# Kernel optimization log

Hardware: AMD Instinct MI355X
Metric: run time of the kernel (lower is better)

Reference implementation:

```python
import jax, jax.numpy as jnp
import numpy as np

B, N, D, H = 8, 1024, 512, 512  # batch, nodes/graph, input dim, hidden/output dim
NEG_SLOPE = 0.2


def _gatv2_layer(x, src, dst, Wl, bl, Wr, br, a, bias, nseg):
    """PyG GATv2Conv (heads=1, add_self_loops=False, eval mode -> no dropout).
    message j->i: alpha_ij = softmax_i( a . leaky_relu(xl[j] + xr[i]) ); out[i] = sum_j alpha_ij * xl[j] + bias
    """
    xl = x @ Wl + bl              # [nseg, H] source transform
    xr = x @ Wr + br              # [nseg, H] target transform
    e = jax.nn.leaky_relu(xl[src] + xr[dst], NEG_SLOPE) @ a  # [E] raw scores
    m = jax.lax.stop_gradient(jax.ops.segment_max(e, dst, num_segments=nseg))
    ex = jnp.exp(e - m[dst])
    s = jax.ops.segment_sum(ex, dst, num_segments=nseg)
    alpha = ex / s[dst]                                       # segment softmax over incoming edges
    out = jax.ops.segment_sum(alpha[:, None] * xl[src], dst, num_segments=nseg)
    return out + bias


def setup_inputs() -> dict:
    key = jax.random.key(0)
    rng = np.random.RandomState(0)
    # random per-graph adjacency, avg degree ~16; block-diagonal edge extraction
    adj_np = (rng.rand(B, N, N) < (16.0 / N))
    srcs, dsts = [], []
    for b in range(B):  # matches torch.nonzero(big_adj).t(): row=src, col=dst
        r, c = np.nonzero(adj_np[b])
        srcs.append(r + b * N)
        dsts.append(c + b * N)
    edge_index = jnp.asarray(np.stack([np.concatenate(srcs), np.concatenate(dsts)]).astype(np.int32))

    ks = jax.random.split(key, 32)
    def lin(k, fi, fo):
        return (jax.random.normal(k, (fi, fo), jnp.float32) / np.sqrt(fi)).astype(jnp.float32)
    inp = {
        "batch_graph": jax.random.normal(ks[0], (B, N, D), jnp.float32),
        "adj": jnp.asarray(adj_np.astype(np.float32)),
        "edge_index": edge_index,
    }
    dims = [(D, H), (H, H), (H, H)]
    for i, (fi, fo) in enumerate(dims, start=1):
        k = jax.random.split(ks[i], 6)
        inp[f"Wl{i}"] = lin(k[0], fi, fo)
        inp[f"bl{i}"] = jnp.zeros((fo,), jnp.float32)
        inp[f"Wr{i}"] = lin(k[1], fi, fo)
        inp[f"br{i}"] = jnp.zeros((fo,), jnp.float32)
        inp[f"a{i}"] = (jax.random.normal(k[2], (fo,), jnp.float32) / np.sqrt(fo)).astype(jnp.float32)
        inp[f"bias{i}"] = jnp.zeros((fo,), jnp.float32)
    return inp


def reference(batch_graph, adj, edge_index,
              Wl1, bl1, Wr1, br1, a1, bias1,
              Wl2, bl2, Wr2, br2, a2, bias2,
              Wl3, bl3, Wr3, br3, a3, bias3):
    b, n, d = batch_graph.shape
    nseg = b * n
    x = batch_graph.reshape(nseg, d)
    src, dst = edge_index[0], edge_index[1]
    x = _gatv2_layer(x, src, dst, Wl1, bl1, Wr1, br1, a1, bias1, nseg)  # graph_norm = Identity
    x = _gatv2_layer(x, src, dst, Wl2, bl2, Wr2, br2, a2, bias2, nseg)
    x = _gatv2_layer(x, src, dst, Wl3, bl3, Wr3, br3, a3, bias3, nseg)
    return x.reshape(b, n, -1)
```

## Files before the change

kernel.cpp:

```cpp
#include <hip/hip_runtime.h>
#include <math.h>

#define MTOT 8192
#define HD   512

typedef __attribute__((ext_vector_type(8))) short bf16x8;
typedef __attribute__((ext_vector_type(4))) float floatx4;
typedef __attribute__((ext_vector_type(4))) float f32x4;
typedef __attribute__((ext_vector_type(4))) unsigned short u16x4;

__device__ inline unsigned short f2bf(float f) {
    unsigned int u = __float_as_uint(f);
    unsigned int r = (u + 0x7FFFu + ((u >> 16) & 1u)) >> 16;
    return (unsigned short)r;
}
__device__ inline float bf2f(unsigned short h) {
    return __uint_as_float(((unsigned int)h) << 16);
}

__device__ inline void nt_st4(float* p, float4 v) {
    f32x4 t = {v.x, v.y, v.z, v.w};
    __builtin_nontemporal_store(t, (f32x4*)p);
}
__device__ inline void nt_stu4(unsigned short* p, ushort4 v) {
    u16x4 t = {v.x, v.y, v.z, v.w};
    __builtin_nontemporal_store(t, (u16x4*)p);
}
__device__ inline float4 nt_ld4(const float* p) {
    f32x4 v = __builtin_nontemporal_load((const f32x4*)p);
    return make_float4(v.x, v.y, v.z, v.w);
}

__device__ inline float wave_sum64(float v) {
    int t;
    t = __builtin_amdgcn_update_dpp(0, __float_as_int(v), 0x121, 0xF, 0xF, true); v += __int_as_float(t);
    t = __builtin_amdgcn_update_dpp(0, __float_as_int(v), 0x122, 0xF, 0xF, true); v += __int_as_float(t);
    t = __builtin_amdgcn_update_dpp(0, __float_as_int(v), 0x124, 0xF, 0xF, true); v += __int_as_float(t);
    t = __builtin_amdgcn_update_dpp(0, __float_as_int(v), 0x128, 0xF, 0xF, true); v += __int_as_float(t);
    v += __shfl_xor(v, 16, 64);
    v += __shfl_xor(v, 32, 64);
    return v;
}


__global__ void count_deg(const int* __restrict__ dst, int* __restrict__ deg, int E) {
    int i = blockIdx.x * 256 + threadIdx.x;
    if (i < E) atomicAdd(&deg[dst[i]], 1);
}

__global__ __launch_bounds__(1024) void scan_offsets(const int* __restrict__ deg,
                                                     int* __restrict__ offs,
                                                     int* __restrict__ cursor) {
    __shared__ int part[1024];
    int tid = threadIdx.x;
    int base = tid * 8;
    int v[8]; int s = 0;
    #pragma unroll
    for (int i = 0; i < 8; ++i) { v[i] = deg[base + i]; s += v[i]; }
    part[tid] = s;
    __syncthreads();
    for (int off = 1; off < 1024; off <<= 1) {
        int t = (tid >= off) ? part[tid - off] : 0;
        __syncthreads();
        part[tid] += t;
        __syncthreads();
    }
    int run = (tid == 0) ? 0 : part[tid - 1];
    #pragma unroll
    for (int i = 0; i < 8; ++i) {
        offs[base + i] = run;
        cursor[base + i] = run;
        run += v[i];
    }
    if (tid == 1023) offs[MTOT] = run;
}

__global__ void scatter_edges(const int* __restrict__ src, const int* __restrict__ dst,
                              int* __restrict__ cursor, int* __restrict__ csr_src, int E) {
    int i = blockIdx.x * 256 + threadIdx.x;
    if (i < E) {
        int p = atomicAdd(&cursor[dst[i]], 1);
        csr_src[p] = src[i];
    }
}


__global__ __launch_bounds__(256) void prep_convert(
    const float* __restrict__ W0, const float* __restrict__ W1,
    const float* __restrict__ W2, const float* __restrict__ W3,
    const float* __restrict__ W4, const float* __restrict__ W5,
    unsigned short* __restrict__ wtbase,
    const float* __restrict__ X,
    unsigned short* __restrict__ Ahi, unsigned short* __restrict__ Alo,
    int* __restrict__ deg)
{
    int z = blockIdx.z;
    if (z == 7) {
        if (blockIdx.x == 0 && blockIdx.y == 0)
            for (int i = threadIdx.x; i < MTOT; i += 256) deg[i] = 0;
        return;
    }
    if (z == 6) {
        int bid = blockIdx.x * 16 + blockIdx.y;
        int t0 = bid * 256 + threadIdx.x;
        #pragma unroll
        for (int it = 0; it < 16; ++it) {
            int i = (t0 + it * 65536) * 4;
            float4 vv = *(const float4*)(X + i);
            ushort4 h, l;
            h.x = f2bf(vv.x); l.x = f2bf(vv.x - bf2f(h.x));
            h.y = f2bf(vv.y); l.y = f2bf(vv.y - bf2f(h.y));
            h.z = f2bf(vv.z); l.z = f2bf(vv.z - bf2f(h.z));
            h.w = f2bf(vv.w); l.w = f2bf(vv.w - bf2f(h.w));
            *(ushort4*)(Ahi + i) = h;
            *(ushort4*)(Alo + i) = l;
        }
        return;
    }
    const float* W = (z == 0) ? W0 : (z == 1) ? W1 : (z == 2) ? W2
                   : (z == 3) ? W3 : (z == 4) ? W4 : W5;
    int L = z >> 1, lr = z & 1;
    const size_t SZ = (size_t)HD * HD;
    unsigned short* Whi = wtbase + (L * 4 + lr * 2) * SZ;
    unsigned short* Wlo = Whi + SZ;

    __shared__ float t[32][33];
    int bx = blockIdx.x * 32;
    int by = blockIdx.y * 32;
    int tx = threadIdx.x & 31, ty = threadIdx.x >> 5;
    for (int i = ty; i < 32; i += 8)
        t[i][tx] = W[(size_t)(by + i) * HD + bx + tx];
    __syncthreads();
    for (int i = ty; i < 32; i += 8) {
        float vv = t[tx][i];
        unsigned short h = f2bf(vv);
        unsigned short l = f2bf(vv - bf2f(h));
        Whi[(size_t)(bx + i) * HD + by + tx] = h;
        Wlo[(size_t)(bx + i) * HD + by + tx] = l;
    }
}


__global__ __launch_bounds__(256) void gemm_mfma_dual(
    const unsigned short* __restrict__ Ahi, const unsigned short* __restrict__ Alo,
    const unsigned short* __restrict__ Bhi_l, const unsigned short* __restrict__ Blo_l,
    const unsigned short* __restrict__ Bhi_r, const unsigned short* __restrict__ Blo_r,
    const float* __restrict__ bias_l, const float* __restrict__ bias_r,
    float* __restrict__ Cl, float* __restrict__ Cr)
{
    int bid = blockIdx.x;
    int virt = (bid & 7) * 64 + (bid >> 3);
    int g  = virt >> 3;
    int q  = virt & 7;
    int bz = q >> 2;
    int bm = g * 128, bn = (q & 3) * 128;

    const unsigned short* Bhi = bz ? Bhi_r : Bhi_l;
    const unsigned short* Blo = bz ? Blo_r : Blo_l;
    const float* bias         = bz ? bias_r : bias_l;
    float* C                  = bz ? Cr : Cl;

    __shared__ __align__(16) unsigned short lds[2][4 * 128 * 32];

    int tid = threadIdx.x;
    int wave = tid >> 6, lane = tid & 63;

    const unsigned short* gsrc[4] = {Ahi, Alo, Bhi, Blo};
    int rowbase[4] = {bm, bm, bn, bn};

    const unsigned short* gbase =
        gsrc[wave] + (size_t)(rowbase[wave] + (lane >> 2)) * 512 + (lane & 3) * 8;

    floatx4 acc[4][4] = {};

    int wm = wave & 1, wn = wave >> 1;
    int lr = lane & 15, lq = lane >> 4;

    #pragma unroll
    for (int rg = 0; rg < 8; ++rg) {
        __builtin_amdgcn_global_load_lds(
            (const __attribute__((address_space(1))) unsigned int*)(gbase + (size_t)rg * 16 * 512),
            (__attribute__((address_space(3))) unsigned int*)(&lds[0][wave * 4096 + rg * 512]),
            16, 0, 0);
    }
    __syncthreads();

    for (int it = 0; it < 16; ++it) {
        int cur = it & 1;
        if (it < 15) {
            const unsigned short* g2 = gbase + (it + 1) * 32;
            #pragma unroll
            for (int rg = 0; rg < 8; ++rg) {
                __builtin_amdgcn_global_load_lds(
                    (const __attribute__((address_space(1))) unsigned int*)(g2 + (size_t)rg * 16 * 512),
                    (__attribute__((address_space(3))) unsigned int*)(&lds[cur ^ 1][wave * 4096 + rg * 512]),
                    16, 0, 0);
            }
        }

        bf16x8 ah[4], al[4], bh[4], bl_[4];
        #pragma unroll
        for (int i = 0; i < 4; ++i) {
            int mrow = wm * 64 + i * 16 + lr;
            ah[i]  = *(const bf16x8*)&lds[cur][0 * 4096 + mrow * 32 + lq * 8];
            al[i]  = *(const bf16x8*)&lds[cur][1 * 4096 + mrow * 32 + lq * 8];
            int nrow = wn * 64 + i * 16 + lr;
            bh[i]  = *(const bf16x8*)&lds[cur][2 * 4096 + nrow * 32 + lq * 8];
            bl_[i] = *(const bf16x8*)&lds[cur][3 * 4096 + nrow * 32 + lq * 8];
        }
        #pragma unroll
        for (int i = 0; i < 4; ++i)
            #pragma unroll
            for (int j = 0; j < 4; ++j) {
                acc[i][j] = __builtin_amdgcn_mfma_f32_16x16x32_bf16(ah[i], bh[j],  acc[i][j], 0, 0, 0);
                acc[i][j] = __builtin_amdgcn_mfma_f32_16x16x32_bf16(ah[i], bl_[j], acc[i][j], 0, 0, 0);
                acc[i][j] = __builtin_amdgcn_mfma_f32_16x16x32_bf16(al[i], bh[j],  acc[i][j], 0, 0, 0);
            }

        __syncthreads();
    }

    #pragma unroll
    for (int j = 0; j < 4; ++j) {
        int n = bn + wn * 64 + j * 16 + lr;
        float bv = bias[n];
        #pragma unroll
        for (int i = 0; i < 4; ++i) {
            int mbase = bm + wm * 64 + i * 16 + lq * 4;
            #pragma unroll
            for (int r = 0; r < 4; ++r)
                C[(size_t)(mbase + r) * 512 + n] = acc[i][j][r] + bv;
        }
    }
}


#define DOT8(Xa, Xb, d0, d1)                                              \
    {                                                                     \
        float t_;                                                         \
        t_ = Xa.x + r0.x; d0 = fmaf(av0.x, t_, d0); d1 = fmaf(av0.x, fabsf(t_), d1); \
        t_ = Xa.y + r0.y; d0 = fmaf(av0.y, t_, d0); d1 = fmaf(av0.y, fabsf(t_), d1); \
        t_ = Xa.z + r0.z; d0 = fmaf(av0.z, t_, d0); d1 = fmaf(av0.z, fabsf(t_), d1); \
        t_ = Xa.w + r0.w; d0 = fmaf(av0.w, t_, d0); d1 = fmaf(av0.w, fabsf(t_), d1); \
        t_ = Xb.x + r1.x; d0 = fmaf(av1.x, t_, d0); d1 = fmaf(av1.x, fabsf(t_), d1); \
        t_ = Xb.y + r1.y; d0 = fmaf(av1.y, t_, d0); d1 = fmaf(av1.y, fabsf(t_), d1); \
        t_ = Xb.z + r1.z; d0 = fmaf(av1.z, t_, d0); d1 = fmaf(av1.z, fabsf(t_), d1); \
        t_ = Xb.w + r1.w; d0 = fmaf(av1.w, t_, d0); d1 = fmaf(av1.w, fabsf(t_), d1); \
    }

#define PROCESS4(Xa, Xb, q)                                               \
    {                                                                     \
        float pe[4];                                                      \
        _Pragma("unroll")                                                 \
        for (int k2 = 0; k2 < 4; ++k2) {                                  \
            float d0 = 0.f, d1 = 0.f;                                     \
            DOT8(Xa[k2], Xb[k2], d0, d1);                                 \
            pe[k2] = fmaf(0.6f, d0, 0.4f * d1);                           \
        }                                                                 \
        _Pragma("unroll")                                                 \
        for (int k2 = 0; k2 < 4; ++k2) pe[k2] = wave_sum64(pe[k2]);       \
        float e0 = pe[0];                                                 \
        float e1 = ((q) + 1 < ne) ? pe[1] : -3.0e38f;                     \
        float e2 = ((q) + 2 < ne) ? pe[2] : -3.0e38f;                     \
        float e3 = ((q) + 3 < ne) ? pe[3] : -3.0e38f;                     \
        float bm4 = fmaxf(fmaxf(e0, e1), fmaxf(e2, e3));                  \
        if (bm4 > m) {                                                    \
            float sc = __expf(m - bm4);                                   \
            s *= sc;                                                      \
            acc0.x *= sc; acc0.y *= sc; acc0.z *= sc; acc0.w *= sc;       \
            acc1.x *= sc; acc1.y *= sc; acc1.z *= sc; acc1.w *= sc;       \
            m = bm4;                                                      \
        }                                                                 \
        float w0 = __expf(e0 - m), w1 = __expf(e1 - m);                   \
        float w2 = __expf(e2 - m), w3 = __expf(e3 - m);                   \
        s += (w0 + w1) + (w2 + w3);                                       \
        acc0.x = fmaf(w0, Xa[0].x, fmaf(w1, Xa[1].x, fmaf(w2, Xa[2].x, fmaf(w3, Xa[3].x, acc0.x)))); \
        acc0.y = fmaf(w0, Xa[0].y, fmaf(w1, Xa[1].y, fmaf(w2, Xa[2].y, fmaf(w3, Xa[3].y, acc0.y)))); \
        acc0.z = fmaf(w0, Xa[0].z, fmaf(w1, Xa[1].z, fmaf(w2, Xa[2].z, fmaf(w3, Xa[3].z, acc0.z)))); \
        acc0.w = fmaf(w0, Xa[0].w, fmaf(w1, Xa[1].w, fmaf(w2, Xa[2].w, fmaf(w3, Xa[3].w, acc0.w)))); \
        acc1.x = fmaf(w0, Xb[0].x, fmaf(w1, Xb[1].x, fmaf(w2, Xb[2].x, fmaf(w3, Xb[3].x, acc1.x)))); \
        acc1.y = fmaf(w0, Xb[0].y, fmaf(w1, Xb[1].y, fmaf(w2, Xb[2].y, fmaf(w3, Xb[3].y, acc1.y)))); \
        acc1.z = fmaf(w0, Xb[0].z, fmaf(w1, Xb[1].z, fmaf(w2, Xb[2].z, fmaf(w3, Xb[3].z, acc1.z)))); \
        acc1.w = fmaf(w0, Xb[0].w, fmaf(w1, Xb[1].w, fmaf(w2, Xb[2].w, fmaf(w3, Xb[3].w, acc1.w)))); \
    }

__global__ __launch_bounds__(256, 4) void gat_online(
    const float* __restrict__ xl, const float* __restrict__ xr,
    const float* __restrict__ avec, const float* __restrict__ bias,
    const int* __restrict__ offs, const int* __restrict__ csr_src,
    float* __restrict__ out, unsigned short* __restrict__ Ohi,
    unsigned short* __restrict__ Olo, int write_fp32)
{
    int gid = blockIdx.x;
    int wv = threadIdx.x >> 6, lane = threadIdx.x & 63;
    int node = ((gid & 7) << 10) + ((gid >> 3) << 2) + wv;

    int nb = offs[node], ne = offs[node + 1];

    int jA[4], jB[4];
    int j0 = (nb < ne) ? csr_src[nb] : 0;
    jA[0] = j0;
    #pragma unroll
    for (int k = 1; k < 4; ++k) jA[k] = (nb + k < ne) ? csr_src[nb + k] : j0;
    #pragma unroll
    for (int k = 0; k < 4; ++k) jB[k] = (nb + 4 + k < ne) ? csr_src[nb + 4 + k] : j0;

    size_t loff = (size_t)lane * 8;
    size_t rowoff = (size_t)node * HD + loff;
    float4 r0 = nt_ld4(xr + rowoff);
    float4 r1 = nt_ld4(xr + rowoff + 4);
    float4 av0 = *(const float4*)(avec + loff);
    float4 av1 = *(const float4*)(avec + loff + 4);

    float m = -3.0e38f, s = 0.f;
    float4 acc0 = {0.f, 0.f, 0.f, 0.f}, acc1 = {0.f, 0.f, 0.f, 0.f};

    float4 Aa[4], Ab[4], Ba[4], Bb[4];
    #pragma unroll
    for (int k = 0; k < 4; ++k) {
        const float* xp = xl + (size_t)jA[k] * HD + loff;
        Aa[k] = *(const float4*)xp;
        Ab[k] = *(const float4*)(xp + 4);
    }

    int p = nb;
    if (p < ne) {
        for (;;) {
            #pragma unroll
            for (int k = 0; k < 4; ++k) {
                const float* xp = xl + (size_t)jB[k] * HD + loff;
                Ba[k] = *(const float4*)xp;
                Bb[k] = *(const float4*)(xp + 4);
            }
            {
                int p2 = p + 8;
                #pragma unroll
                for (int k = 0; k < 4; ++k)
                    jA[k] = (p2 + k < ne) ? csr_src[p2 + k] : j0;
            }
            PROCESS4(Aa, Ab, p);
            p += 4;
            if (p >= ne) break;

            #pragma unroll
            for (int k = 0; k < 4; ++k) {
                const float* xp = xl + (size_t)jA[k] * HD + loff;
                Aa[k] = *(const float4*)xp;
                Ab[k] = *(const float4*)(xp + 4);
            }
            {
                int p2 = p + 8;
                #pragma unroll
                for (int k = 0; k < 4; ++k)
                    jB[k] = (p2 + k < ne) ? csr_src[p2 + k] : j0;
            }
            PROCESS4(Ba, Bb, p);
            p += 4;
            if (p >= ne) break;
        }
    }

    float inv = (s > 0.f) ? 1.f / s : 0.f;
    float4 b0 = *(const float4*)(bias + loff);
    float4 b1 = *(const float4*)(bias + loff + 4);
    float4 o0, o1;
    o0.x = fmaf(acc0.x, inv, b0.x); o0.y = fmaf(acc0.y, inv, b0.y);
    o0.z = fmaf(acc0.z, inv, b0.z); o0.w = fmaf(acc0.w, inv, b0.w);
    o1.x = fmaf(acc1.x, inv, b1.x); o1.y = fmaf(acc1.y, inv, b1.y);
    o1.z = fmaf(acc1.z, inv, b1.z); o1.w = fmaf(acc1.w, inv, b1.w);

    if (write_fp32) {
        nt_st4(out + rowoff, o0);
        nt_st4(out + rowoff + 4, o1);
    } else {
        ushort4 h, lo;
        h.x = f2bf(o0.x); lo.x = f2bf(o0.x - bf2f(h.x));
        h.y = f2bf(o0.y); lo.y = f2bf(o0.y - bf2f(h.y));
        h.z = f2bf(o0.z); lo.z = f2bf(o0.z - bf2f(h.z));
        h.w = f2bf(o0.w); lo.w = f2bf(o0.w - bf2f(h.w));
        nt_stu4(Ohi + rowoff, h);
        nt_stu4(Olo + rowoff, lo);
        h.x = f2bf(o1.x); lo.x = f2bf(o1.x - bf2f(h.x));
        h.y = f2bf(o1.y); lo.y = f2bf(o1.y - bf2f(h.y));
        h.z = f2bf(o1.z); lo.z = f2bf(o1.z - bf2f(h.z));
        h.w = f2bf(o1.w); lo.w = f2bf(o1.w - bf2f(h.w));
        nt_stu4(Ohi + rowoff + 4, h);
        nt_stu4(Olo + rowoff + 4, lo);
    }
}


extern "C" void kernel_launch(void* const* d_in, const int* in_sizes, int n_in,
                              void* d_out, int out_size, void* d_ws, size_t ws_size,
                              hipStream_t stream) {
    const float* x0 = (const float*)d_in[0];
    const int* eidx = (const int*)d_in[2];
    int E = in_sizes[2] / 2;
    const int* esrc = eidx;
    const int* edst = eidx + E;

    const float* Wl[3] = {(const float*)d_in[3],  (const float*)d_in[9],  (const float*)d_in[15]};
    const float* bl[3] = {(const float*)d_in[4],  (const float*)d_in[10], (const float*)d_in[16]};
    const float* Wr[3] = {(const float*)d_in[5],  (const float*)d_in[11], (const float*)d_in[17]};
    const float* br[3] = {(const float*)d_in[6],  (const float*)d_in[12], (const float*)d_in[18]};
    const float* av[3] = {(const float*)d_in[7],  (const float*)d_in[13], (const float*)d_in[19]};
    const float* bs[3] = {(const float*)d_in[8],  (const float*)d_in[14], (const float*)d_in[20]};

    char* w = (char*)d_ws;
    unsigned short* Ahi = (unsigned short*)w; w += (size_t)MTOT * HD * 2;
    unsigned short* Alo = (unsigned short*)w; w += (size_t)MTOT * HD * 2;
    unsigned short* wtbase = (unsigned short*)w; w += 12 * (size_t)HD * HD * 2;
    float* xl = (float*)w; w += (size_t)MTOT * HD * 4;
    float* xr = (float*)w; w += (size_t)MTOT * HD * 4;
    int* deg    = (int*)w;
    int* offs   = deg + MTOT;
    int* cursor = offs + MTOT + 8;
    int* csr    = cursor + MTOT;
    const size_t SZ = (size_t)HD * HD;

    prep_convert<<<dim3(16, 16, 8), 256, 0, stream>>>(
        Wl[0], Wr[0], Wl[1], Wr[1], Wl[2], Wr[2], wtbase, x0, Ahi, Alo, deg);
    count_deg<<<(E + 255) / 256, 256, 0, stream>>>(edst, deg, E);
    scan_offsets<<<1, 1024, 0, stream>>>(deg, offs, cursor);
    scatter_edges<<<(E + 255) / 256, 256, 0, stream>>>(esrc, edst, cursor, csr, E);

    for (int L = 0; L < 3; ++L) {
        gemm_mfma_dual<<<512, 256, 0, stream>>>(Ahi, Alo,
            wtbase + (L * 4 + 0) * SZ, wtbase + (L * 4 + 1) * SZ,
            wtbase + (L * 4 + 2) * SZ, wtbase + (L * 4 + 3) * SZ,
            bl[L], br[L], xl, xr);
        int last = (L == 2);
        gat_online<<<MTOT / 4, 256, 0, stream>>>(xl, xr, av[L], bs[L], offs, csr,
                                                 last ? (float*)d_out : nullptr,
                                                 last ? nullptr : Ahi,
                                                 last ? nullptr : Alo,
                                                 last);
    }
}
```

Before: 301.4 us.

## Prefetch two stages ahead in GEMM with explicit vmcnt waits

Restructures the double-buffered GEMM main loop so two K-stages are issued up front and each later stage is launched after compute, two iterations ahead. It uses explicit s_waitcnt vmcnt counts plus raw s_barrier instead of __syncthreads, so only the loads for the current stage must have landed. The goal is deeper overlap of global-to-LDS loads with MFMA work and fewer full-drain waits. It relies on the compiler's vmcnt accounting matching the hand-written counts, and sched_barrier limits instruction reordering.

```diff
diff --git a/kernel.cpp b/kernel.cpp
--- a/kernel.cpp
+++ b/kernel.cpp
@@ -176,27 +176,31 @@
     int wm = wave & 1, wn = wave >> 1;
     int lr = lane & 15, lq = lane >> 4;
 
-    #pragma unroll
-    for (int rg = 0; rg < 8; ++rg) {
-        __builtin_amdgcn_global_load_lds(
-            (const __attribute__((address_space(1))) unsigned int*)(gbase + (size_t)rg * 16 * 512),
-            (__attribute__((address_space(3))) unsigned int*)(&lds[0][wave * 4096 + rg * 512]),
-            16, 0, 0);
-    }
-    __syncthreads();
+#define STAGE16(IT, BUF)                                                      \
+    {                                                                         \
+        const unsigned short* g2_ = gbase + (IT) * 32;                        \
+        _Pragma("unroll")                                                     \
+        for (int rg = 0; rg < 8; ++rg) {                                      \
+            __builtin_amdgcn_global_load_lds(                                 \
+                (const __attribute__((address_space(1))) unsigned int*)(g2_ + (size_t)rg * 16 * 512), \
+                (__attribute__((address_space(3))) unsigned int*)(&lds[BUF][wave * 4096 + rg * 512]), \
+                16, 0, 0);                                                    \
+        }                                                                     \
+    }
+
+    STAGE16(0, 0);
+    STAGE16(1, 1);
 
     for (int it = 0; it < 16; ++it) {
         int cur = it & 1;
+
         if (it < 15) {
-            const unsigned short* g2 = gbase + (it + 1) * 32;
-            #pragma unroll
-            for (int rg = 0; rg < 8; ++rg) {
-                __builtin_amdgcn_global_load_lds(
-                    (const __attribute__((address_space(1))) unsigned int*)(g2 + (size_t)rg * 16 * 512),
-                    (__attribute__((address_space(3))) unsigned int*)(&lds[cur ^ 1][wave * 4096 + rg * 512]),
-                    16, 0, 0);
-            }
+            asm volatile("s_waitcnt vmcnt(8)" ::: "memory");
+        } else {
+            asm volatile("s_waitcnt vmcnt(0)" ::: "memory");
         }
+        __builtin_amdgcn_s_barrier();
+        __builtin_amdgcn_sched_barrier(0);
 
         bf16x8 ah[4], al[4], bh[4], bl_[4];
         #pragma unroll
@@ -217,8 +221,13 @@
                 acc[i][j] = __builtin_amdgcn_mfma_f32_16x16x32_bf16(al[i], bh[j],  acc[i][j], 0, 0, 0);
             }
 
-        __syncthreads();
-    }
+        __builtin_amdgcn_sched_barrier(0);
+        __builtin_amdgcn_s_barrier();
+        __builtin_amdgcn_sched_barrier(0);
+
+        if (it < 14) STAGE16(it + 2, cur);
+    }
+#undef STAGE16
 
     #pragma unroll
     for (int j = 0; j < 4; ++j) {
```

Measured after the change: 306.9 us. About the same (+1.8%).
